# Kernel optimization log

Measured on AMD Instinct MI355X. Metric: run time of the kernel, lower is better.

Reference implementation:

```python
import jax, jax.numpy as jnp
import numpy as np

TEMPERATURE = 12.5   # args.temperature (DeepEMD default)
EPS = 0.05           # entropic regularization for the OT (EMD) solve
N_ITERS = 100        # Sinkhorn iterations
COS_EPS = 1e-8       # F.cosine_similarity eps


def setup_inputs() -> dict:
    key = jax.random.key(0)
    k1, k2 = jax.random.split(key)
    B, C, H, W = 512, 1024, 8, 8
    proto = jax.random.normal(k1, (B, C, H, W), dtype=jnp.float32)
    query = jax.random.normal(k2, (B, C, H, W), dtype=jnp.float32)
    return {"proto": proto, "query": query}


def get_weight_vector(A, Bmap):
    """A,[b,c,h,w]; pooled Bmap reweights A's channels -> node weights [b, h*w]."""
    pooled = Bmap.mean(axis=(2, 3), keepdims=True)          # adaptive_avg_pool2d -> [b,c,1,1]
    comb = (A * pooled).sum(axis=1).reshape(A.shape[0], -1)  # [b, h*w]
    return jax.nn.relu(comb) + 0.001


def center(x):
    # args.norm == 'center': subtract channel mean
    return x - x.mean(axis=1, keepdims=True)


def cosine_sim_map(proto, query):
    """sim[b, q_node, p_node] = cosine similarity between flattened spatial nodes."""
    B, C = proto.shape[0], proto.shape[1]
    p = proto.reshape(B, C, -1).transpose(0, 2, 1)   # [b, Np, c]
    q = query.reshape(B, C, -1).transpose(0, 2, 1)   # [b, Nq, c]
    pn = p / jnp.maximum(jnp.linalg.norm(p, axis=-1, keepdims=True), COS_EPS)
    qn = q / jnp.maximum(jnp.linalg.norm(q, axis=-1, keepdims=True), COS_EPS)
    return jnp.einsum('bqc,bpc->bqp', qn, pn)        # [b, Nq, Np]


def sinkhorn_flow(cost, r, c):
    """Entropic-regularized OT flow with marginals r [b,N], c [b,M]; cost [b,N,M]."""
    K = jnp.exp(-cost / EPS)
    v0 = jnp.ones_like(c)

    def body(v, _):
        u = r / jnp.maximum(jnp.einsum('bnm,bm->bn', K, v), 1e-30)
        v = c / jnp.maximum(jnp.einsum('bnm,bn->bm', K, u), 1e-30)
        return v, None

    v, _ = jax.lax.scan(body, v0, None, length=N_ITERS)
    u = r / jnp.maximum(jnp.einsum('bnm,bm->bn', K, v), 1e-30)
    return u[:, :, None] * K * v[:, None, :]         # [b, N, M]


def reference(proto, query):
    # emd_forward(proto, query)
    weight_1 = get_weight_vector(query, proto)       # [b, Nq]
    weight_2 = get_weight_vector(proto, query)       # [b, Np]
    p = center(proto)
    q = center(query)
    sim = cosine_sim_map(p, q)                       # [b, Nq, Np]
    # get_emd_distance: solve OT on cost = 1 - sim with (normalized) node weights
    r = weight_1 / weight_1.sum(axis=-1, keepdims=True)
    c = weight_2 / weight_2.sum(axis=-1, keepdims=True)
    flow = sinkhorn_flow(1.0 - sim, r, c)
    num_node = weight_1.shape[-1]
    logits = (sim * flow).sum(axis=(-1, -2)) * (TEMPERATURE / num_node)
    return logits
```

## Files before the change

### kernel.cpp

```cpp
#include <hip/hip_runtime.h>
#include <math.h>

#define NCH    1024
#define NN     64
#define CK     32
#define KSC    28.853900817779268f
#define WSB    4352

typedef __attribute__((ext_vector_type(8))) short bf16x8;
typedef __attribute__((ext_vector_type(4))) float f32x4;
typedef union { unsigned int u[4]; bf16x8 v; } FragCvt;

#define STAT_Q(v) { sqp[0]+=(v).x; q2p[0]=fmaf((v).x,(v).x,q2p[0]); \
                    sqp[1]+=(v).y; q2p[1]=fmaf((v).y,(v).y,q2p[1]); \
                    sqp[2]+=(v).z; q2p[2]=fmaf((v).z,(v).z,q2p[2]); \
                    sqp[3]+=(v).w; q2p[3]=fmaf((v).w,(v).w,q2p[3]); }
#define STAT_P(v) { spp[0]+=(v).x; p2p[0]=fmaf((v).x,(v).x,p2p[0]); \
                    spp[1]+=(v).y; p2p[1]=fmaf((v).y,(v).y,p2p[1]); \
                    spp[2]+=(v).z; p2p[2]=fmaf((v).z,(v).z,p2p[2]); \
                    spp[3]+=(v).w; p2p[3]=fmaf((v).w,(v).w,p2p[3]); }

__device__ __forceinline__ float4 ldnt4(const float* p) {
    f32x4 t = __builtin_nontemporal_load((const f32x4*)p);
    float4 r; r.x = t.x; r.y = t.y; r.z = t.z; r.w = t.w;
    return r;
}

__device__ __forceinline__ void cvt2(float x0, float x1,
                                     unsigned int& hw, unsigned int& lw) {
    unsigned int u0 = __float_as_uint(x0), u1 = __float_as_uint(x1);
    unsigned int h0 = (u0 + 0x7FFFu + ((u0 >> 16) & 1u)) & 0xFFFF0000u;
    unsigned int h1 = (u1 + 0x7FFFu + ((u1 >> 16) & 1u)) & 0xFFFF0000u;
    hw = (h0 >> 16) | h1;
    float l0 = x0 - __uint_as_float(h0);
    float l1 = x1 - __uint_as_float(h1);
    lw = (__float_as_uint(l0) >> 16) | (__float_as_uint(l1) & 0xFFFF0000u);
}

__device__ __forceinline__ int ldword(int k, int n) {
    return n * 32 + (k ^ (n & 24));
}

template<int LOGNS>
__global__ __launch_bounds__(256)
void gram_mfma4(const float* __restrict__ proto,
                const float* __restrict__ query,
                float* __restrict__ ws)
{
    constexpr int NCHUNK = 32 >> LOGNS;

    __shared__ __align__(16) char ldsbuf[65536];

    const int w   = threadIdx.x >> 6;
    const int rid = blockIdx.x * 4 + w;
    const int b = rid >> LOGNS, s = rid & ((1 << LOGNS) - 1);
    const int l = threadIdx.x & 63;
    const int lam = l & 15, g = l >> 4;

    float* const ldsQ = (float*)(ldsbuf + w * 16384);
    float* const ldsP = ldsQ + 2048;

    const float* __restrict__ qw = query + (size_t)b * 65536 + s * (65536 >> LOGNS);
    const float* __restrict__ pw = proto + (size_t)b * 65536 + s * (65536 >> LOGNS);

    f32x4 acc[4][4];
    #pragma unroll
    for (int r = 0; r < 4; ++r)
        #pragma unroll
        for (int c = 0; c < 4; ++c) {
            acc[r][c][0] = 0.0f; acc[r][c][1] = 0.0f;
            acc[r][c][2] = 0.0f; acc[r][c][3] = 0.0f;
        }
    float sqp[4] = {0,0,0,0}, q2p[4] = {0,0,0,0};
    float spp[4] = {0,0,0,0}, p2p[4] = {0,0,0,0};

    float4 qv[8], pv[8];
    #pragma unroll
    for (int grp = 0; grp < 8; ++grp) {
        qv[grp] = ldnt4(qw + grp * 256 + 4 * l);
        pv[grp] = ldnt4(pw + grp * 256 + 4 * l);
    }

    #pragma unroll 1
    for (int ch8 = 0; ch8 < NCHUNK; ++ch8) {
        #pragma unroll
        for (int grp = 0; grp < 8; ++grp) {
            STAT_Q(qv[grp]); STAT_P(pv[grp]);
            const int kk = grp * 4 + g;
            const float qe[4] = {qv[grp].x, qv[grp].y, qv[grp].z, qv[grp].w};
            const float pe[4] = {pv[grp].x, pv[grp].y, pv[grp].z, pv[grp].w};
            #pragma unroll
            for (int i = 0; i < 4; ++i) {
                const int n = 4 * lam + i;
                const int wd = ldword(kk, n);
                ldsQ[wd] = qe[i];
                ldsP[wd] = pe[i];
            }
        }
        if (ch8 + 1 < NCHUNK) {
            #pragma unroll
            for (int grp = 0; grp < 8; ++grp) {
                qv[grp] = ldnt4(qw + (ch8 + 1) * 2048 + grp * 256 + 4 * l);
                pv[grp] = ldnt4(pw + (ch8 + 1) * 2048 + grp * 256 + 4 * l);
            }
        }
        __builtin_amdgcn_sched_barrier(0);

        unsigned int bh[4][4], bl[4][4];
        #pragma unroll
        for (int c = 0; c < 4; ++c) {
            const int n = c * 16 + lam;
            const int w0 = ldword(8 * g, n);
            float4 x0 = *(const float4*)(ldsP + w0);
            float4 x1 = *(const float4*)(ldsP + w0 + 4);
            cvt2(x0.x, x0.y, bh[c][0], bl[c][0]);
            cvt2(x0.z, x0.w, bh[c][1], bl[c][1]);
            cvt2(x1.x, x1.y, bh[c][2], bl[c][2]);
            cvt2(x1.z, x1.w, bh[c][3], bl[c][3]);
        }
        #pragma unroll
        for (int r = 0; r < 4; ++r) {
            const int n = r * 16 + lam;
            const int w0 = ldword(8 * g, n);
            float4 x0 = *(const float4*)(ldsQ + w0);
            float4 x1 = *(const float4*)(ldsQ + w0 + 4);
            FragCvt ah, al;
            cvt2(x0.x, x0.y, ah.u[0], al.u[0]);
            cvt2(x0.z, x0.w, ah.u[1], al.u[1]);
            cvt2(x1.x, x1.y, ah.u[2], al.u[2]);
            cvt2(x1.z, x1.w, ah.u[3], al.u[3]);
            #pragma unroll
            for (int c = 0; c < 4; ++c) {
                FragCvt bhv, blv;
                bhv.u[0] = bh[c][0]; bhv.u[1] = bh[c][1];
                bhv.u[2] = bh[c][2]; bhv.u[3] = bh[c][3];
                blv.u[0] = bl[c][0]; blv.u[1] = bl[c][1];
                blv.u[2] = bl[c][2]; blv.u[3] = bl[c][3];
                acc[r][c] = __builtin_amdgcn_mfma_f32_16x16x32_bf16(ah.v, bhv.v, acc[r][c], 0, 0, 0);
                acc[r][c] = __builtin_amdgcn_mfma_f32_16x16x32_bf16(ah.v, blv.v, acc[r][c], 0, 0, 0);
                acc[r][c] = __builtin_amdgcn_mfma_f32_16x16x32_bf16(al.v, bhv.v, acc[r][c], 0, 0, 0);
            }
        }
    }

    #pragma unroll
    for (int k = 0; k < 4; ++k) {
        sqp[k] += __shfl_xor(sqp[k], 16, 64); sqp[k] += __shfl_xor(sqp[k], 32, 64);
        q2p[k] += __shfl_xor(q2p[k], 16, 64); q2p[k] += __shfl_xor(q2p[k], 32, 64);
        spp[k] += __shfl_xor(spp[k], 16, 64); spp[k] += __shfl_xor(spp[k], 32, 64);
        p2p[k] += __shfl_xor(p2p[k], 16, 64); p2p[k] += __shfl_xor(p2p[k], 32, 64);
    }

    float* __restrict__ wsb = ws + (size_t)rid * WSB;
    #pragma unroll
    for (int r = 0; r < 4; ++r)
        #pragma unroll
        for (int c = 0; c < 4; ++c)
            #pragma unroll
            for (int i = 0; i < 4; ++i)
                wsb[(r * 16 + 4 * g + i) * 64 + c * 16 + lam] = acc[r][c][i];
    if (l < 16) {
        #pragma unroll
        for (int k = 0; k < 4; ++k) {
            wsb[4096 +   0 + 4 * lam + k] = sqp[k];
            wsb[4096 +  64 + 4 * lam + k] = q2p[k];
            wsb[4096 + 128 + 4 * lam + k] = spp[k];
            wsb[4096 + 192 + 4 * lam + k] = p2p[k];
        }
    }
}

#define DOT16(KK, ARR) ({ \
    float4 x0 = *(const float4*)&ARR[sp4*16 +  0]; \
    float4 x1 = *(const float4*)&ARR[sp4*16 +  4]; \
    float4 x2 = *(const float4*)&ARR[sp4*16 +  8]; \
    float4 x3 = *(const float4*)&ARR[sp4*16 + 12]; \
    float a0 = 0.0f, a1 = 0.0f; \
    a0=fmaf(KK[0],x0.x,a0);  a1=fmaf(KK[1],x0.y,a1); \
    a0=fmaf(KK[2],x0.z,a0);  a1=fmaf(KK[3],x0.w,a1); \
    a0=fmaf(KK[4],x1.x,a0);  a1=fmaf(KK[5],x1.y,a1); \
    a0=fmaf(KK[6],x1.z,a0);  a1=fmaf(KK[7],x1.w,a1); \
    a0=fmaf(KK[8],x2.x,a0);  a1=fmaf(KK[9],x2.y,a1); \
    a0=fmaf(KK[10],x2.z,a0); a1=fmaf(KK[11],x2.w,a1); \
    a0=fmaf(KK[12],x3.x,a0); a1=fmaf(KK[13],x3.y,a1); \
    a0=fmaf(KK[14],x3.z,a0); a1=fmaf(KK[15],x3.w,a1); \
    a0 + a1; })

template<int NS>
__global__ __launch_bounds__(256)
void emd_solve(const float* __restrict__ ws, float* __restrict__ out)
{
    __shared__ __align__(16) float stage[16 * 64];
    __shared__ __align__(16) float Kl [NN][68];
    __shared__ __align__(16) float KTl[NN][68];
    __shared__ __align__(16) float statL[4][NN];
    __shared__ __align__(16) float uL[NN];
    __shared__ __align__(16) float vL[NN];
    __shared__ __align__(16) float rL[NN];
    __shared__ __align__(16) float cL[NN];
    __shared__ float redl[4];

    const int b  = blockIdx.x;
    const int t  = threadIdx.x;
    const int tr = t >> 4, tc = t & 15;
    const int n0 = tr * 4, m0 = tc * 4;

    const float* __restrict__ wsb = ws + (size_t)b * NS * WSB;

    float acc[4][4];
    #pragma unroll
    for (int i = 0; i < 4; ++i)
        #pragma unroll
        for (int j = 0; j < 4; ++j) acc[i][j] = 0.0f;
    #pragma unroll
    for (int s = 0; s < NS; ++s) {
        const float* __restrict__ g = wsb + s * WSB;
        #pragma unroll
        for (int i = 0; i < 4; ++i) {
            float4 v = *(const float4*)&g[(n0 + i) * 64 + m0];
            acc[i][0] += v.x; acc[i][1] += v.y; acc[i][2] += v.z; acc[i][3] += v.w;
        }
    }
    if (t < NN) {
        float s0 = 0, s1 = 0, s2 = 0, s3 = 0;
        #pragma unroll
        for (int s = 0; s < NS; ++s) {
            const float* __restrict__ g = wsb + s * WSB + 4096;
            s0 += g[t]; s1 += g[64 + t]; s2 += g[128 + t]; s3 += g[192 + t];
        }
        statL[0][t] = s0; statL[1][t] = s1; statL[2][t] = s2; statL[3][t] = s3;
    }
    #pragma unroll
    for (int i = 0; i < 4; ++i) {
        float s = acc[i][0] + acc[i][1] + acc[i][2] + acc[i][3];
        s += __shfl_xor(s, 1, 64); s += __shfl_xor(s, 2, 64);
        s += __shfl_xor(s, 4, 64); s += __shfl_xor(s, 8, 64);
        if (tc == 0) uL[n0 + i] = s;
    }
    #pragma unroll
    for (int j = 0; j < 4; ++j)
        stage[tr * 64 + m0 + j] = acc[0][j] + acc[1][j] + acc[2][j] + acc[3][j];
    __syncthreads();

    if (t < NN) {
        float cs = 0;
        #pragma unroll
        for (int i = 0; i < 16; ++i) cs += stage[i * 64 + t];
        float w2 = fmaxf(cs * (1.0f/64.0f), 0.0f) + 0.001f;
        float w1 = fmaxf(uL[t] * (1.0f/64.0f), 0.0f) + 0.001f;
        float s1 = w1, s2 = w2;
        #pragma unroll
        for (int m = 1; m < 64; m <<= 1) {
            s1 += __shfl_xor(s1, m, 64);
            s2 += __shfl_xor(s2, m, 64);
        }
        rL[t] = w1 / s1;
        cL[t] = w2 / s2;
        vL[t] = 1.0f;
    }
    {
        float nq_[4], np_[4], sqn[4], spm[4];
        #pragma unroll
        for (int i = 0; i < 4; ++i) {
            float sv  = statL[0][n0 + i];
            float var = statL[1][n0 + i] - sv * sv * (1.0f/1024.0f);
            nq_[i] = fmaxf(sqrtf(fmaxf(var, 0.0f)), 1e-8f);
            sqn[i] = sv;
        }
        #pragma unroll
        for (int j = 0; j < 4; ++j) {
            float sv  = statL[2][m0 + j];
            float var = statL[3][m0 + j] - sv * sv * (1.0f/1024.0f);
            np_[j] = fmaxf(sqrtf(fmaxf(var, 0.0f)), 1e-8f);
            spm[j] = sv;
        }
        #pragma unroll
        for (int i = 0; i < 4; ++i) {
            #pragma unroll
            for (int j = 0; j < 4; ++j) {
                float sim = (acc[i][j] - sqn[i] * spm[j] * (1.0f/1024.0f)) / (nq_[i] * np_[j]);
                acc[i][j] = sim;
                float Kv = exp2f((sim - 1.0f) * KSC);
                Kl [n0 + i][m0 + j] = Kv;
                KTl[m0 + j][n0 + i] = Kv;
            }
        }
    }
    __syncthreads();

    const int sn  = t >> 2;
    const int sp4 = t & 3;
    float Kr[16], KTr[16];
    #pragma unroll
    for (int jj = 0; jj < 4; ++jj) {
        float4 kv = *(const float4*)&Kl [sn][sp4 * 16 + jj * 4];
        float4 kt = *(const float4*)&KTl[sn][sp4 * 16 + jj * 4];
        Kr [jj*4+0]=kv.x; Kr [jj*4+1]=kv.y; Kr [jj*4+2]=kv.z; Kr [jj*4+3]=kv.w;
        KTr[jj*4+0]=kt.x; KTr[jj*4+1]=kt.y; KTr[jj*4+2]=kt.z; KTr[jj*4+3]=kt.w;
    }
    const float rreg = rL[sn];
    const float creg = cL[sn];

    for (int it = 0; it < 100; ++it) {
        float s = DOT16(Kr, vL);
        s += __shfl_xor(s, 1, 64); s += __shfl_xor(s, 2, 64);
        float u = rreg / fmaxf(s, 1e-30f);
        if (sp4 == 0) uL[sn] = u;
        __syncthreads();
        float s2 = DOT16(KTr, uL);
        s2 += __shfl_xor(s2, 1, 64); s2 += __shfl_xor(s2, 2, 64);
        float vv = creg / fmaxf(s2, 1e-30f);
        if (sp4 == 0) vL[sn] = vv;
        __syncthreads();
    }
    {
        float s = DOT16(Kr, vL);
        s += __shfl_xor(s, 1, 64); s += __shfl_xor(s, 2, 64);
        float u = rreg / fmaxf(s, 1e-30f);
        if (sp4 == 0) uL[sn] = u;
    }
    __syncthreads();

    float uu[4], vv_[4];
    #pragma unroll
    for (int i = 0; i < 4; ++i) uu[i]  = uL[n0 + i];
    #pragma unroll
    for (int j = 0; j < 4; ++j) vv_[j] = vL[m0 + j];
    float part = 0.0f;
    #pragma unroll
    for (int i = 0; i < 4; ++i) {
        #pragma unroll
        for (int j = 0; j < 4; ++j) {
            float sim = acc[i][j];
            float Kv  = exp2f((sim - 1.0f) * KSC);
            part = fmaf(sim * Kv, uu[i] * vv_[j], part);
        }
    }
    #pragma unroll
    for (int m = 1; m < 64; m <<= 1) part += __shfl_xor(part, m, 64);
    if ((t & 63) == 0) redl[t >> 6] = part;
    __syncthreads();
    if (t == 0) out[b] = (redl[0] + redl[1] + redl[2] + redl[3]) * (12.5f / 64.0f);
}

#define STAT_QF(v) { sqp[0]+=(v).x; q2p[0]=fmaf((v).x,(v).x,q2p[0]); \
                     sqp[1]+=(v).y; q2p[1]=fmaf((v).y,(v).y,q2p[1]); \
                     sqp[2]+=(v).z; q2p[2]=fmaf((v).z,(v).z,q2p[2]); \
                     sqp[3]+=(v).w; q2p[3]=fmaf((v).w,(v).w,q2p[3]); }
#define STAT_PF(v) { spp[0]+=(v).x; p2p[0]=fmaf((v).x,(v).x,p2p[0]); \
                     spp[1]+=(v).y; p2p[1]=fmaf((v).y,(v).y,p2p[1]); \
                     spp[2]+=(v).z; p2p[2]=fmaf((v).z,(v).z,p2p[2]); \
                     spp[3]+=(v).w; p2p[3]=fmaf((v).w,(v).w,p2p[3]); }

__global__ __launch_bounds__(256)
void deepemd_fused(const float* __restrict__ proto,
                   const float* __restrict__ query,
                   float* __restrict__ out)
{
    __shared__ __align__(16) float stage[2 * CK * NN];
    __shared__ __align__(16) float Kl [NN][68];
    __shared__ __align__(16) float KTl[NN][68];
    __shared__ __align__(16) float statL[4][NN];
    __shared__ __align__(16) float uL[NN];
    __shared__ __align__(16) float vL[NN];
    __shared__ __align__(16) float rL[NN];
    __shared__ __align__(16) float cL[NN];
    __shared__ float redl[4];

    const int b  = blockIdx.x;
    const int t  = threadIdx.x;
    const int tr = t >> 4, tc = t & 15;
    const int n0 = tr * 4, m0 = tc * 4;
    const int ofs = 4 * t;

    const float* __restrict__ pb = proto + (size_t)b * (NCH * NN);
    const float* __restrict__ qb = query + (size_t)b * (NCH * NN);

    float acc[4][4];
    #pragma unroll
    for (int i = 0; i < 4; ++i)
        #pragma unroll
        for (int j = 0; j < 4; ++j) acc[i][j] = 0.0f;
    float sqp[4] = {0,0,0,0}, q2p[4] = {0,0,0,0};
    float spp[4] = {0,0,0,0}, p2p[4] = {0,0,0,0};

    float4 qv0 = *(const float4*)(qb + ofs);
    float4 qv1 = *(const float4*)(qb + 1024 + ofs);
    float4 pv0 = *(const float4*)(pb + ofs);
    float4 pv1 = *(const float4*)(pb + 1024 + ofs);

    for (int ch = 0; ch < NCH / CK; ++ch) {
        if (ch) __syncthreads();
        *(float4*)&stage[       ofs] = qv0;
        *(float4*)&stage[1024 + ofs] = qv1;
        *(float4*)&stage[2048 + ofs] = pv0;
        *(float4*)&stage[3072 + ofs] = pv1;
        float4 nq0, nq1, np0, np1;
        const bool more = (ch + 1 < NCH / CK);
        if (more) {
            const float* qn = qb + (ch + 1) * 2048;
            const float* pn = pb + (ch + 1) * 2048;
            nq0 = *(const float4*)(qn + ofs);
            nq1 = *(const float4*)(qn + 1024 + ofs);
            np0 = *(const float4*)(pn + ofs);
            np1 = *(const float4*)(pn + 1024 + ofs);
        }
        STAT_QF(qv0); STAT_QF(qv1);
        STAT_PF(pv0); STAT_PF(pv1);
        __syncthreads();
        #pragma unroll 8
        for (int cc = 0; cc < CK; ++cc) {
            float4 a  = *(const float4*)&stage[cc * 64 + n0];
            float4 bb = *(const float4*)&stage[2048 + cc * 64 + m0];
            acc[0][0]=fmaf(a.x,bb.x,acc[0][0]); acc[0][1]=fmaf(a.x,bb.y,acc[0][1]);
            acc[0][2]=fmaf(a.x,bb.z,acc[0][2]); acc[0][3]=fmaf(a.x,bb.w,acc[0][3]);
            acc[1][0]=fmaf(a.y,bb.x,acc[1][0]); acc[1][1]=fmaf(a.y,bb.y,acc[1][1]);
            acc[1][2]=fmaf(a.y,bb.z,acc[1][2]); acc[1][3]=fmaf(a.y,bb.w,acc[1][3]);
            acc[2][0]=fmaf(a.z,bb.x,acc[2][0]); acc[2][1]=fmaf(a.z,bb.y,acc[2][1]);
            acc[2][2]=fmaf(a.z,bb.z,acc[2][2]); acc[2][3]=fmaf(a.z,bb.w,acc[2][3]);
            acc[3][0]=fmaf(a.w,bb.x,acc[3][0]); acc[3][1]=fmaf(a.w,bb.y,acc[3][1]);
            acc[3][2]=fmaf(a.w,bb.z,acc[3][2]); acc[3][3]=fmaf(a.w,bb.w,acc[3][3]);
        }
        if (more) { qv0 = nq0; qv1 = nq1; pv0 = np0; pv1 = np1; }
    }
    __syncthreads();

    #pragma unroll
    for (int i = 0; i < 4; ++i) {
        float s = acc[i][0] + acc[i][1] + acc[i][2] + acc[i][3];
        s += __shfl_xor(s, 1, 64); s += __shfl_xor(s, 2, 64);
        s += __shfl_xor(s, 4, 64); s += __shfl_xor(s, 8, 64);
        if (tc == 0) uL[n0 + i] = s;
    }
    #pragma unroll
    for (int k = 0; k < 4; ++k) {
        stage[t*16 +      k] = sqp[k];
        stage[t*16 +  4 + k] = q2p[k];
        stage[t*16 +  8 + k] = spp[k];
        stage[t*16 + 12 + k] = p2p[k];
    }
    __syncthreads();
    if (t < NN) {
        const int g = t >> 2, k = t & 3;
        float ssq = 0, sq2 = 0, ssp = 0, sp2 = 0;
        #pragma unroll
        for (int j = 0; j < 16; ++j) {
            const float* row = &stage[(j * 16 + g) * 16];
            ssq += row[k]; sq2 += row[4 + k]; ssp += row[8 + k]; sp2 += row[12 + k];
        }
        statL[0][t] = ssq; statL[1][t] = sq2; statL[2][t] = ssp; statL[3][t] = sp2;
    }
    __syncthreads();
    #pragma unroll
    for (int j = 0; j < 4; ++j)
        stage[tr * 64 + m0 + j] = acc[0][j] + acc[1][j] + acc[2][j] + acc[3][j];
    __syncthreads();
    if (t < NN) {
        float cs = 0;
        #pragma unroll
        for (int i = 0; i < 16; ++i) cs += stage[i * 64 + t];
        float w2 = fmaxf(cs * (1.0f/64.0f), 0.0f) + 0.001f;
        float w1 = fmaxf(uL[t] * (1.0f/64.0f), 0.0f) + 0.001f;
        float s1 = w1, s2 = w2;
        #pragma unroll
        for (int m = 1; m < 64; m <<= 1) {
            s1 += __shfl_xor(s1, m, 64);
            s2 += __shfl_xor(s2, m, 64);
        }
        rL[t] = w1 / s1;
        cL[t] = w2 / s2;
        vL[t] = 1.0f;
    }
    __syncthreads();

    {
        float nq_[4], np_[4], sqn[4], spm[4];
        #pragma unroll
        for (int i = 0; i < 4; ++i) {
            float sv  = statL[0][n0 + i];
            float var = statL[1][n0 + i] - sv * sv * (1.0f/1024.0f);
            nq_[i] = fmaxf(sqrtf(fmaxf(var, 0.0f)), 1e-8f);
            sqn[i] = sv;
        }
        #pragma unroll
        for (int j = 0; j < 4; ++j) {
            float sv  = statL[2][m0 + j];
            float var = statL[3][m0 + j] - sv * sv * (1.0f/1024.0f);
            np_[j] = fmaxf(sqrtf(fmaxf(var, 0.0f)), 1e-8f);
            spm[j] = sv;
        }
        #pragma unroll
        for (int i = 0; i < 4; ++i) {
            #pragma unroll
            for (int j = 0; j < 4; ++j) {
                float sim = (acc[i][j] - sqn[i] * spm[j] * (1.0f/1024.0f)) / (nq_[i] * np_[j]);
                acc[i][j] = sim;
                float Kv = exp2f((sim - 1.0f) * KSC);
                Kl [n0 + i][m0 + j] = Kv;
                KTl[m0 + j][n0 + i] = Kv;
            }
        }
    }
    __syncthreads();

    const int sn  = t >> 2;
    const int sp4 = t & 3;
    float Kr[16], KTr[16];
    #pragma unroll
    for (int jj = 0; jj < 4; ++jj) {
        float4 kv = *(const float4*)&Kl [sn][sp4 * 16 + jj * 4];
        float4 kt = *(const float4*)&KTl[sn][sp4 * 16 + jj * 4];
        Kr [jj*4+0]=kv.x; Kr [jj*4+1]=kv.y; Kr [jj*4+2]=kv.z; Kr [jj*4+3]=kv.w;
        KTr[jj*4+0]=kt.x; KTr[jj*4+1]=kt.y; KTr[jj*4+2]=kt.z; KTr[jj*4+3]=kt.w;
    }
    const float rreg = rL[sn];
    const float creg = cL[sn];

    for (int it = 0; it < 100; ++it) {
        float s = DOT16(Kr, vL);
        s += __shfl_xor(s, 1, 64); s += __shfl_xor(s, 2, 64);
        float u = rreg / fmaxf(s, 1e-30f);
        if (sp4 == 0) uL[sn] = u;
        __syncthreads();
        float s2 = DOT16(KTr, uL);
        s2 += __shfl_xor(s2, 1, 64); s2 += __shfl_xor(s2, 2, 64);
        float vv = creg / fmaxf(s2, 1e-30f);
        if (sp4 == 0) vL[sn] = vv;
        __syncthreads();
    }
    {
        float s = DOT16(Kr, vL);
        s += __shfl_xor(s, 1, 64); s += __shfl_xor(s, 2, 64);
        float u = rreg / fmaxf(s, 1e-30f);
        if (sp4 == 0) uL[sn] = u;
    }
    __syncthreads();

    float uu[4], vv_[4];
    #pragma unroll
    for (int i = 0; i < 4; ++i) uu[i]  = uL[n0 + i];
    #pragma unroll
    for (int j = 0; j < 4; ++j) vv_[j] = vL[m0 + j];
    float part = 0.0f;
    #pragma unroll
    for (int i = 0; i < 4; ++i) {
        #pragma unroll
        for (int j = 0; j < 4; ++j) {
            float sim = acc[i][j];
            float Kv  = exp2f((sim - 1.0f) * KSC);
            part = fmaf(sim * Kv, uu[i] * vv_[j], part);
        }
    }
    #pragma unroll
    for (int m = 1; m < 64; m <<= 1) part += __shfl_xor(part, m, 64);
    if ((t & 63) == 0) redl[t >> 6] = part;
    __syncthreads();
    if (t == 0) out[b] = (redl[0] + redl[1] + redl[2] + redl[3]) * (12.5f / 64.0f);
}

extern "C" void kernel_launch(void* const* d_in, const int* in_sizes, int n_in,
                              void* d_out, int out_size, void* d_ws, size_t ws_size,
                              hipStream_t stream) {
    const float* proto = (const float*)d_in[0];
    const float* query = (const float*)d_in[1];
    float* out = (float*)d_out;
    (void)in_sizes; (void)n_in; (void)out_size;

    const size_t need4 = (size_t)512 * 4 * WSB * sizeof(float);
    if (ws_size >= need4) {
        gram_mfma4<2><<<dim3(512 * 4 / 4), dim3(256), 0, stream>>>(proto, query, (float*)d_ws);
        emd_solve<4><<<dim3(512),          dim3(256), 0, stream>>>((const float*)d_ws, out);
    } else {
        deepemd_fused<<<dim3(512), dim3(256), 0, stream>>>(proto, query, out);
    }
}
```

Before: 119.8 us.

## Solve Sinkhorn with one wavefront per batch, K rows held in registers

```diff
diff --git a/kernel.cpp b/kernel.cpp
--- a/kernel.cpp
+++ b/kernel.cpp
@@ -170,6 +170,143 @@
     }
 }
 
+template<int NS>
+__global__ __launch_bounds__(64)
+void emd_solve1w(const float* __restrict__ ws, float* __restrict__ out)
+{
+    __shared__ __align__(16) float T[64 * 65];
+    __shared__ float SQ[NN], NQ[NN], SP[NN], NP[NN];
+    __shared__ __align__(16) float uL[NN];
+    __shared__ __align__(16) float vL[NN];
+
+    const int b = blockIdx.x;
+    const int l = threadIdx.x;
+    const float* __restrict__ wsb = ws + (size_t)b * NS * WSB;
+
+    float G[64];
+    #pragma unroll
+    for (int m = 0; m < 64; ++m) G[m] = 0.0f;
+    #pragma unroll 1
+    for (int s = 0; s < NS; ++s) {
+        const float* __restrict__ g = wsb + s * WSB;
+        #pragma unroll
+        for (int i = 0; i < 16; ++i) {
+            float4 v = *(const float4*)(g + i * 256 + 4 * l);
+            const int e = i * 256 + 4 * l;
+            *(float4*)&T[(e >> 6) * 65 + (e & 63)] = v;
+        }
+        #pragma unroll
+        for (int i = 0; i < 16; ++i) {
+            float4 x = *(const float4*)&T[l * 65 + 4 * i];
+            G[4*i+0] += x.x; G[4*i+1] += x.y; G[4*i+2] += x.z; G[4*i+3] += x.w;
+        }
+    }
+    float sq = 0, q2 = 0, sp = 0, p2 = 0;
+    #pragma unroll
+    for (int s = 0; s < NS; ++s) {
+        const float* __restrict__ g = wsb + s * WSB + 4096;
+        sq += g[l]; q2 += g[64 + l]; sp += g[128 + l]; p2 += g[192 + l];
+    }
+    float nq = fmaxf(sqrtf(fmaxf(q2 - sq * sq * (1.0f/1024.0f), 0.0f)), 1e-8f);
+    float np = fmaxf(sqrtf(fmaxf(p2 - sp * sp * (1.0f/1024.0f), 0.0f)), 1e-8f);
+    SQ[l] = sq; NQ[l] = nq; SP[l] = sp; NP[l] = np;
+
+    #pragma unroll
+    for (int i = 0; i < 16; ++i) {
+        float4 x; x.x = G[4*i+0]; x.y = G[4*i+1]; x.z = G[4*i+2]; x.w = G[4*i+3];
+        *(float4*)&T[l * 65 + 4 * i] = x;
+    }
+
+    float rs = 0.0f;
+    #pragma unroll
+    for (int i = 0; i < 16; ++i)
+        rs += (G[4*i+0] + G[4*i+1]) + (G[4*i+2] + G[4*i+3]);
+
+    float KT[64];
+    float cs = 0.0f;
+    #pragma unroll
+    for (int m = 0; m < 64; ++m) {
+        float gv = T[m * 65 + l];
+        cs += gv;
+        float simT = (gv - SQ[m] * sp * (1.0f/1024.0f)) / (NQ[m] * np);
+        KT[m] = exp2f((simT - 1.0f) * KSC);
+    }
+
+    float w1 = fmaxf(rs * (1.0f/64.0f), 0.0f) + 0.001f;
+    float w2 = fmaxf(cs * (1.0f/64.0f), 0.0f) + 0.001f;
+    float s1 = w1, s2 = w2;
+    #pragma unroll
+    for (int m = 1; m < 64; m <<= 1) {
+        s1 += __shfl_xor(s1, m, 64);
+        s2 += __shfl_xor(s2, m, 64);
+    }
+    const float rl = w1 / s1;
+    const float cl = w2 / s2;
+
+    float Krow[64];
+    #pragma unroll
+    for (int m = 0; m < 64; ++m) {
+        float sim = (G[m] - sq * SP[m] * (1.0f/1024.0f)) / (nq * NP[m]);
+        Krow[m] = exp2f((sim - 1.0f) * KSC);
+    }
+
+    vL[l] = 1.0f;
+
+#define MATVEC(KK, ARR, OUTV) do {                                  \
+        float a0 = 0.0f, a1 = 0.0f, a2 = 0.0f, a3 = 0.0f;           \
+        _Pragma("unroll")                                           \
+        for (int mm = 0; mm < 16; ++mm) {                           \
+            float4 vv = *(const float4*)&ARR[4 * mm];               \
+            a0 = fmaf(KK[4*mm+0], vv.x, a0);                        \
+            a1 = fmaf(KK[4*mm+1], vv.y, a1);                        \
+            a2 = fmaf(KK[4*mm+2], vv.z, a2);                        \
+            a3 = fmaf(KK[4*mm+3], vv.w, a3);                        \
+        }                                                           \
+        OUTV = (a0 + a1) + (a2 + a3);                               \
+    } while (0)
+
+    float u;
+    #pragma unroll 1
+    for (int it = 0; it < 100; ++it) {
+        float kv; MATVEC(Krow, vL, kv);
+        u = rl / fmaxf(kv, 1e-30f);
+        uL[l] = u;
+        float ku; MATVEC(KT, uL, ku);
+        float v = cl / fmaxf(ku, 1e-30f);
+        vL[l] = v;
+    }
+    { float kv; MATVEC(Krow, vL, kv); u = rl / fmaxf(kv, 1e-30f); }
+#undef MATVEC
+
+    float part = 0.0f;
+    #pragma unroll
+    for (int i = 0; i < 16; ++i) {
+        float4 gx = *(const float4*)&T[l * 65 + 4 * i];
+        float4 vv = *(const float4*)&vL[4 * i];
+        const float ge[4] = {gx.x, gx.y, gx.z, gx.w};
+        const float ve[4] = {vv.x, vv.y, vv.z, vv.w};
+        #pragma unroll
+        for (int j = 0; j < 4; ++j) {
+            const int m = 4 * i + j;
+            float sim = (ge[j] - sq * SP[m] * (1.0f/1024.0f)) / (nq * NP[m]);
+            part = fmaf(sim * Krow[m], ve[j], part);
+        }
+    }
+    part *= u;
+    #pragma unroll
+    for (int m = 1; m < 64; m <<= 1) part += __shfl_xor(part, m, 64);
+    if (l == 0) out[b] = part * (12.5f / 64.0f);
+}
+
+#define STAT_QF(v) { sqp[0]+=(v).x; q2p[0]=fmaf((v).x,(v).x,q2p[0]); \
+                     sqp[1]+=(v).y; q2p[1]=fmaf((v).y,(v).y,q2p[1]); \
+                     sqp[2]+=(v).z; q2p[2]=fmaf((v).z,(v).z,q2p[2]); \
+                     sqp[3]+=(v).w; q2p[3]=fmaf((v).w,(v).w,q2p[3]); }
+#define STAT_PF(v) { spp[0]+=(v).x; p2p[0]=fmaf((v).x,(v).x,p2p[0]); \
+                     spp[1]+=(v).y; p2p[1]=fmaf((v).y,(v).y,p2p[1]); \
+                     spp[2]+=(v).z; p2p[2]=fmaf((v).z,(v).z,p2p[2]); \
+                     spp[3]+=(v).w; p2p[3]=fmaf((v).w,(v).w,p2p[3]); }
+
 #define DOT16(KK, ARR) ({ \
     float4 x0 = *(const float4*)&ARR[sp4*16 +  0]; \
     float4 x1 = *(const float4*)&ARR[sp4*16 +  4]; \
@@ -186,172 +323,6 @@
     a0=fmaf(KK[14],x3.z,a0); a1=fmaf(KK[15],x3.w,a1); \
     a0 + a1; })
 
-template<int NS>
-__global__ __launch_bounds__(256)
-void emd_solve(const float* __restrict__ ws, float* __restrict__ out)
-{
-    __shared__ __align__(16) float stage[16 * 64];
-    __shared__ __align__(16) float Kl [NN][68];
-    __shared__ __align__(16) float KTl[NN][68];
-    __shared__ __align__(16) float statL[4][NN];
-    __shared__ __align__(16) float uL[NN];
-    __shared__ __align__(16) float vL[NN];
-    __shared__ __align__(16) float rL[NN];
-    __shared__ __align__(16) float cL[NN];
-    __shared__ float redl[4];
-
-    const int b  = blockIdx.x;
-    const int t  = threadIdx.x;
-    const int tr = t >> 4, tc = t & 15;
-    const int n0 = tr * 4, m0 = tc * 4;
-
-    const float* __restrict__ wsb = ws + (size_t)b * NS * WSB;
-
-    float acc[4][4];
-    #pragma unroll
-    for (int i = 0; i < 4; ++i)
-        #pragma unroll
-        for (int j = 0; j < 4; ++j) acc[i][j] = 0.0f;
-    #pragma unroll
-    for (int s = 0; s < NS; ++s) {
-        const float* __restrict__ g = wsb + s * WSB;
-        #pragma unroll
-        for (int i = 0; i < 4; ++i) {
-            float4 v = *(const float4*)&g[(n0 + i) * 64 + m0];
-            acc[i][0] += v.x; acc[i][1] += v.y; acc[i][2] += v.z; acc[i][3] += v.w;
-        }
-    }
-    if (t < NN) {
-        float s0 = 0, s1 = 0, s2 = 0, s3 = 0;
-        #pragma unroll
-        for (int s = 0; s < NS; ++s) {
-            const float* __restrict__ g = wsb + s * WSB + 4096;
-            s0 += g[t]; s1 += g[64 + t]; s2 += g[128 + t]; s3 += g[192 + t];
-        }
-        statL[0][t] = s0; statL[1][t] = s1; statL[2][t] = s2; statL[3][t] = s3;
-    }
-    #pragma unroll
-    for (int i = 0; i < 4; ++i) {
-        float s = acc[i][0] + acc[i][1] + acc[i][2] + acc[i][3];
-        s += __shfl_xor(s, 1, 64); s += __shfl_xor(s, 2, 64);
-        s += __shfl_xor(s, 4, 64); s += __shfl_xor(s, 8, 64);
-        if (tc == 0) uL[n0 + i] = s;
-    }
-    #pragma unroll
-    for (int j = 0; j < 4; ++j)
-        stage[tr * 64 + m0 + j] = acc[0][j] + acc[1][j] + acc[2][j] + acc[3][j];
-    __syncthreads();
-
-    if (t < NN) {
-        float cs = 0;
-        #pragma unroll
-        for (int i = 0; i < 16; ++i) cs += stage[i * 64 + t];
-        float w2 = fmaxf(cs * (1.0f/64.0f), 0.0f) + 0.001f;
-        float w1 = fmaxf(uL[t] * (1.0f/64.0f), 0.0f) + 0.001f;
-        float s1 = w1, s2 = w2;
-        #pragma unroll
-        for (int m = 1; m < 64; m <<= 1) {
-            s1 += __shfl_xor(s1, m, 64);
-            s2 += __shfl_xor(s2, m, 64);
-        }
-        rL[t] = w1 / s1;
-        cL[t] = w2 / s2;
-        vL[t] = 1.0f;
-    }
-    {
-        float nq_[4], np_[4], sqn[4], spm[4];
-        #pragma unroll
-        for (int i = 0; i < 4; ++i) {
-            float sv  = statL[0][n0 + i];
-            float var = statL[1][n0 + i] - sv * sv * (1.0f/1024.0f);
-            nq_[i] = fmaxf(sqrtf(fmaxf(var, 0.0f)), 1e-8f);
-            sqn[i] = sv;
-        }
-        #pragma unroll
-        for (int j = 0; j < 4; ++j) {
-            float sv  = statL[2][m0 + j];
-            float var = statL[3][m0 + j] - sv * sv * (1.0f/1024.0f);
-            np_[j] = fmaxf(sqrtf(fmaxf(var, 0.0f)), 1e-8f);
-            spm[j] = sv;
-        }
-        #pragma unroll
-        for (int i = 0; i < 4; ++i) {
-            #pragma unroll
-            for (int j = 0; j < 4; ++j) {
-                float sim = (acc[i][j] - sqn[i] * spm[j] * (1.0f/1024.0f)) / (nq_[i] * np_[j]);
-                acc[i][j] = sim;
-                float Kv = exp2f((sim - 1.0f) * KSC);
-                Kl [n0 + i][m0 + j] = Kv;
-                KTl[m0 + j][n0 + i] = Kv;
-            }
-        }
-    }
-    __syncthreads();
-
-    const int sn  = t >> 2;
-    const int sp4 = t & 3;
-    float Kr[16], KTr[16];
-    #pragma unroll
-    for (int jj = 0; jj < 4; ++jj) {
-        float4 kv = *(const float4*)&Kl [sn][sp4 * 16 + jj * 4];
-        float4 kt = *(const float4*)&KTl[sn][sp4 * 16 + jj * 4];
-        Kr [jj*4+0]=kv.x; Kr [jj*4+1]=kv.y; Kr [jj*4+2]=kv.z; Kr [jj*4+3]=kv.w;
-        KTr[jj*4+0]=kt.x; KTr[jj*4+1]=kt.y; KTr[jj*4+2]=kt.z; KTr[jj*4+3]=kt.w;
-    }
-    const float rreg = rL[sn];
-    const float creg = cL[sn];
-
-    for (int it = 0; it < 100; ++it) {
-        float s = DOT16(Kr, vL);
-        s += __shfl_xor(s, 1, 64); s += __shfl_xor(s, 2, 64);
-        float u = rreg / fmaxf(s, 1e-30f);
-        if (sp4 == 0) uL[sn] = u;
-        __syncthreads();
-        float s2 = DOT16(KTr, uL);
-        s2 += __shfl_xor(s2, 1, 64); s2 += __shfl_xor(s2, 2, 64);
-        float vv = creg / fmaxf(s2, 1e-30f);
-        if (sp4 == 0) vL[sn] = vv;
-        __syncthreads();
-    }
-    {
-        float s = DOT16(Kr, vL);
-        s += __shfl_xor(s, 1, 64); s += __shfl_xor(s, 2, 64);
-        float u = rreg / fmaxf(s, 1e-30f);
-        if (sp4 == 0) uL[sn] = u;
-    }
-    __syncthreads();
-
-    float uu[4], vv_[4];
-    #pragma unroll
-    for (int i = 0; i < 4; ++i) uu[i]  = uL[n0 + i];
-    #pragma unroll
-    for (int j = 0; j < 4; ++j) vv_[j] = vL[m0 + j];
-    float part = 0.0f;
-    #pragma unroll
-    for (int i = 0; i < 4; ++i) {
-        #pragma unroll
-        for (int j = 0; j < 4; ++j) {
-            float sim = acc[i][j];
-            float Kv  = exp2f((sim - 1.0f) * KSC);
-            part = fmaf(sim * Kv, uu[i] * vv_[j], part);
-        }
-    }
-    #pragma unroll
-    for (int m = 1; m < 64; m <<= 1) part += __shfl_xor(part, m, 64);
-    if ((t & 63) == 0) redl[t >> 6] = part;
-    __syncthreads();
-    if (t == 0) out[b] = (redl[0] + redl[1] + redl[2] + redl[3]) * (12.5f / 64.0f);
-}
-
-#define STAT_QF(v) { sqp[0]+=(v).x; q2p[0]=fmaf((v).x,(v).x,q2p[0]); \
-                     sqp[1]+=(v).y; q2p[1]=fmaf((v).y,(v).y,q2p[1]); \
-                     sqp[2]+=(v).z; q2p[2]=fmaf((v).z,(v).z,q2p[2]); \
-                     sqp[3]+=(v).w; q2p[3]=fmaf((v).w,(v).w,q2p[3]); }
-#define STAT_PF(v) { spp[0]+=(v).x; p2p[0]=fmaf((v).x,(v).x,p2p[0]); \
-                     spp[1]+=(v).y; p2p[1]=fmaf((v).y,(v).y,p2p[1]); \
-                     spp[2]+=(v).z; p2p[2]=fmaf((v).z,(v).z,p2p[2]); \
-                     spp[3]+=(v).w; p2p[3]=fmaf((v).w,(v).w,p2p[3]); }
-
 __global__ __launch_bounds__(256)
 void deepemd_fused(const float* __restrict__ proto,
                    const float* __restrict__ query,
@@ -569,7 +540,7 @@
     const size_t need4 = (size_t)512 * 4 * WSB * sizeof(float);
     if (ws_size >= need4) {
         gram_mfma4<2><<<dim3(512 * 4 / 4), dim3(256), 0, stream>>>(proto, query, (float*)d_ws);
-        emd_solve<4><<<dim3(512),          dim3(256), 0, stream>>>((const float*)d_ws, out);
+        emd_solve1w<4><<<dim3(512),        dim3(64),  0, stream>>>((const float*)d_ws, out);
     } else {
         deepemd_fused<<<dim3(512), dim3(256), 0, stream>>>(proto, query, out);
     }
```

Result: slower. 149.1 us (+24.5%).
